# Kernel optimization log

Hardware: AMD Instinct MI355X
Metric: run time of the kernel (lower is better)

## Reference

```python
import jax, jax.numpy as jnp
import numpy as np

B, S, D, H = 4, 2048, 1024, 16
HD = D // H  # head_dim = 64


def setup_inputs() -> dict:
    key = jax.random.key(0)
    k1, k2, k3 = jax.random.split(key, 3)
    scale = 0.02
    return {
        "hidden_states": jax.random.normal(k1, (B, S, D), dtype=jnp.float32),
        "W_attn": jax.random.normal(k2, (D, 3 * D), dtype=jnp.float32) * scale,
        "b_attn": jnp.zeros((3 * D,), dtype=jnp.float32),
        "W_proj": jax.random.normal(k3, (D, D), dtype=jnp.float32) * scale,
        "b_proj": jnp.zeros((D,), dtype=jnp.float32),
    }


def reference(hidden_states, W_attn, b_attn, W_proj, b_proj):
    b, s, d = hidden_states.shape
    qkv = hidden_states @ W_attn + b_attn  # [B,S,3D]
    q, k, v = jnp.split(qkv, 3, axis=-1)
    # [B,S,D] -> [B,H,S,hd]
    def to_heads(x):
        return x.reshape(b, s, H, HD).transpose(0, 2, 1, 3)
    q, k, v = to_heads(q), to_heads(k), to_heads(v)
    scores = jnp.einsum("bhqd,bhkd->bhqk", q, k) / jnp.sqrt(jnp.float32(HD))
    causal = jnp.tril(jnp.ones((s, s), dtype=bool))  # [S,S]
    scores = jnp.where(causal[None, None], scores, jnp.float32(-jnp.inf))
    probs = jax.nn.softmax(scores, axis=-1)  # dropout p=0 -> identity (eval)
    out = jnp.einsum("bhqk,bhkd->bhqd", probs, v)  # [B,H,S,hd]
    out = out.transpose(0, 2, 1, 3).reshape(b, s, d)
    return out @ W_proj + b_proj
```

## Files before the change

kernel.cpp:

```cpp
#include <hip/hip_runtime.h>
#include <hip/hip_bf16.h>


typedef float f32x4 __attribute__((ext_vector_type(4)));
typedef __bf16 bf16x8 __attribute__((ext_vector_type(8)));
typedef unsigned short u16x8 __attribute__((ext_vector_type(8)));
typedef unsigned short u16x4 __attribute__((ext_vector_type(4)));

static constexpr int Sq = 2048, Dm = 1024, HD = 64, N3 = 3072;
static constexpr int Mrows = 4 * Sq;
static constexpr float SM_SCALE = 0.18033688011112042f;
static constexpr float SM_BIAS  = -11.541560327111707f;

__device__ __forceinline__ float bf2f(unsigned short u) {
  union { unsigned u32; float f; } x; x.u32 = ((unsigned)u) << 16; return x.f;
}
__device__ __forceinline__ unsigned short f2bf(float f) {
  return __builtin_bit_cast(unsigned short, (__bf16)f);
}
__device__ __forceinline__ f32x4 mfma16(u16x8 a, u16x8 b, f32x4 c) {
  return __builtin_amdgcn_mfma_f32_16x16x32_bf16(
      __builtin_bit_cast(bf16x8, a), __builtin_bit_cast(bf16x8, b), c, 0, 0, 0);
}

__global__ __launch_bounds__(256) void cvt_k(
    const float* __restrict__ in, unsigned short* __restrict__ out, int n) {
  int stride = gridDim.x * 256 * 4;
  for (int i = (blockIdx.x * 256 + threadIdx.x) * 4; i < n; i += stride) {
    f32x4 v = *reinterpret_cast<const f32x4*>(&in[i]);
    u16x4 o;
    #pragma unroll
    for (int j = 0; j < 4; j++) o[j] = f2bf(v[j]);
    *reinterpret_cast<u16x4*>(&out[i]) = o;
  }
}

__global__ __launch_bounds__(256) void tcvt_k(
    const float* __restrict__ in, unsigned short* __restrict__ out,
    int R, int C) {
  __shared__ float tile[32][33];
  int c0 = blockIdx.x * 32, r0 = blockIdx.y * 32;
  int tx = threadIdx.x & 31, ty = threadIdx.x >> 5;
  #pragma unroll
  for (int i = 0; i < 32; i += 8)
    tile[ty + i][tx] = in[(size_t)(r0 + ty + i) * C + c0 + tx];
  __syncthreads();
  #pragma unroll
  for (int i = 0; i < 32; i += 8)
    out[(size_t)(c0 + ty + i) * R + r0 + tx] = f2bf(tile[tx][ty + i]);
}

template <bool OUT_F32>
__global__ __launch_bounds__(256) void gemm_bt(
    const unsigned short* __restrict__ A, const unsigned short* __restrict__ Bt,
    const float* __restrict__ bias, void* __restrict__ Cout,
    int Md, int Nd, int Kd) {
  __shared__ unsigned short Asm[128 * 32];
  __shared__ unsigned short Bsm[128 * 32];
  int t = threadIdx.x;
  int wave = t >> 6, lane = t & 63;
  int lrow = lane & 15, lq = lane >> 4;
  int wr = wave >> 1, wc = wave & 1;
  int bm = blockIdx.y * 128, bn = blockIdx.x * 128;
  f32x4 acc[4][4] = {};

  for (int k0 = 0; k0 < Kd; k0 += 32) {
    __syncthreads();
    #pragma unroll
    for (int c = 0; c < 2; c++) {
      int e = c * 2048 + t * 8;
      int row = e >> 5, col = e & 31;
      const unsigned short* ga = A + (size_t)(bm + row) * Kd + k0 + col;
      const unsigned short* gb = Bt + (size_t)(bn + row) * Kd + k0 + col;
      __builtin_amdgcn_global_load_lds(
          (const __attribute__((address_space(1))) void*)ga,
          (__attribute__((address_space(3))) void*)((char*)Asm + c * 4096 + wave * 1024),
          16, 0, 0);
      __builtin_amdgcn_global_load_lds(
          (const __attribute__((address_space(1))) void*)gb,
          (__attribute__((address_space(3))) void*)((char*)Bsm + c * 4096 + wave * 1024),
          16, 0, 0);
    }
    __syncthreads();

    u16x8 af[4], bfr[4];
    #pragma unroll
    for (int m = 0; m < 4; m++)
      af[m] = *reinterpret_cast<const u16x8*>(&Asm[(wr * 64 + m * 16 + lrow) * 32 + lq * 8]);
    #pragma unroll
    for (int n = 0; n < 4; n++)
      bfr[n] = *reinterpret_cast<const u16x8*>(&Bsm[(wc * 64 + n * 16 + lrow) * 32 + lq * 8]);
    #pragma unroll
    for (int m = 0; m < 4; m++)
      #pragma unroll
      for (int n = 0; n < 4; n++)
        acc[m][n] = mfma16(af[m], bfr[n], acc[m][n]);
  }

  #pragma unroll
  for (int n = 0; n < 4; n++) {
    int col = bn + wc * 64 + n * 16 + lrow;
    float bv = bias[col];
    #pragma unroll
    for (int m = 0; m < 4; m++) {
      #pragma unroll
      for (int j = 0; j < 4; j++) {
        int row = bm + wr * 64 + m * 16 + lq * 4 + j;
        if constexpr (OUT_F32)
          ((float*)Cout)[(size_t)row * Nd + col] = acc[m][n][j] + bv;
        else
          ((unsigned short*)Cout)[(size_t)row * Nd + col] = f2bf(acc[m][n][j] + bv);
      }
    }
  }
}

__global__ __launch_bounds__(256) void attn_k(
    const unsigned short* __restrict__ qkv,
    unsigned short* __restrict__ ao) {
  int bh = blockIdx.y;
  int b = bh >> 4, h = bh & 15;
  int t = threadIdx.x, wave = t >> 6, lane = t & 63;
  int lrow = lane & 15, lq = lane >> 4;

  __shared__ unsigned short Kl[2][64][72];
  __shared__ unsigned short Vt[2][64][72];
  __shared__ unsigned short Pl[4][16][72];

  const size_t base = (size_t)b * Sq * N3;
  const unsigned short* Kbase = qkv + base + Dm + h * HD;
  const unsigned short* Vbase = qkv + base + 2 * Dm + h * HD;

  int irow = t >> 2, icol = (t & 3) * 16;
  int vd = lane, vkb = wave;

  u16x8 ones;
  #pragma unroll
  for (int j = 0; j < 8; j++) ones[j] = 0x3F80;

  u16x8 kr0, kr1, vr0, vr1;
  auto prefetch = [&](int kv) {
    const unsigned short* kp = Kbase + (size_t)(kv + irow) * N3 + icol;
    kr0 = *reinterpret_cast<const u16x8*>(kp);
    kr1 = *reinterpret_cast<const u16x8*>(kp + 8);
    const unsigned short* vp = Vbase + (size_t)kv * N3 + vd;
    #pragma unroll
    for (int i = 0; i < 8; i++) {
      vr0[i] = vp[(size_t)(vkb * 8 + i) * N3];
      vr1[i] = vp[(size_t)(32 + vkb * 8 + i) * N3];
    }
  };

  #pragma unroll 1
  for (int pass = 0; pass < 2; ++pass) {
    int qb = pass ? (int)blockIdx.x : 15 - (int)blockIdx.x;
    int q0 = qb * 128;
    int ntiles = 2 * qb + 2;
    int rw0 = q0 + wave * 32;

    u16x8 qf[2][2];
    #pragma unroll
    for (int m = 0; m < 2; m++) {
      const unsigned short* qp =
          qkv + base + (size_t)(rw0 + m * 16 + lrow) * N3 + h * HD + lq * 8;
      u16x8 r0 = *reinterpret_cast<const u16x8*>(qp);
      u16x8 r1 = *reinterpret_cast<const u16x8*>(qp + 32);
      #pragma unroll
      for (int j = 0; j < 8; j++) {
        qf[m][0][j] = f2bf(SM_SCALE * bf2f(r0[j]));
        qf[m][1][j] = f2bf(SM_SCALE * bf2f(r1[j]));
      }
    }

    f32x4 oacc[2][4] = {};
    f32x4 dacc[2] = {};

    if (pass == 0) prefetch(0);

    #pragma unroll 1
    for (int kt = 0; kt < ntiles; ++kt) {
      int kv = kt * 64, bsel = kt & 1;
      *reinterpret_cast<u16x8*>(&Kl[bsel][irow][icol]) = kr0;
      *reinterpret_cast<u16x8*>(&Kl[bsel][irow][icol + 8]) = kr1;
      *reinterpret_cast<u16x8*>(&Vt[bsel][vd][vkb * 8]) = vr0;
      *reinterpret_cast<u16x8*>(&Vt[bsel][vd][32 + vkb * 8]) = vr1;
      if (kt + 1 < ntiles) prefetch(kv + 64);
      else if (pass == 0) prefetch(0);
      __syncthreads();

      u16x8 kf0[4], kf1[4];
      #pragma unroll
      for (int ct = 0; ct < 4; ct++) {
        kf0[ct] = *reinterpret_cast<const u16x8*>(&Kl[bsel][ct * 16 + lrow][lq * 8]);
        kf1[ct] = *reinterpret_cast<const u16x8*>(&Kl[bsel][ct * 16 + lrow][32 + lq * 8]);
      }
      f32x4 sacc[2][4];
      #pragma unroll
      for (int m = 0; m < 2; m++)
        #pragma unroll
        for (int ct = 0; ct < 4; ct++)
          sacc[m][ct] = f32x4{SM_BIAS, SM_BIAS, SM_BIAS, SM_BIAS};
      __builtin_amdgcn_s_setprio(1);
      #pragma unroll
      for (int m = 0; m < 2; m++)
        #pragma unroll
        for (int ct = 0; ct < 4; ct++) {
          sacc[m][ct] = mfma16(kf0[ct], qf[m][0], sacc[m][ct]);
          sacc[m][ct] = mfma16(kf1[ct], qf[m][1], sacc[m][ct]);
        }
      __builtin_amdgcn_s_setprio(0);

      u16x8 vf0[4], vf1[4];
      #pragma unroll
      for (int ht = 0; ht < 4; ht++) {
        vf0[ht] = *reinterpret_cast<const u16x8*>(&Vt[bsel][ht * 16 + lrow][lq * 8]);
        vf1[ht] = *reinterpret_cast<const u16x8*>(&Vt[bsel][ht * 16 + lrow][32 + lq * 8]);
      }

      #pragma unroll
      for (int m = 0; m < 2; m++) {
        int rwm = rw0 + m * 16;
        bool need_mask = kv + 63 > rwm;
        int dlim = rwm - kv + lrow;
        #pragma unroll
        for (int ct = 0; ct < 4; ct++) {
          u16x4 o;
          #pragma unroll
          for (int j = 0; j < 4; j++) {
            float e = exp2f(sacc[m][ct][j]);
            if (need_mask) e = (16 * ct + 4 * lq + j <= dlim) ? e : 0.f;
            o[j] = f2bf(e);
          }
          *reinterpret_cast<u16x4*>(&Pl[wave][lrow][16 * ct + 4 * lq]) = o;
        }

        u16x8 pa0 = *reinterpret_cast<const u16x8*>(&Pl[wave][lrow][lq * 8]);
        u16x8 pa1 = *reinterpret_cast<const u16x8*>(&Pl[wave][lrow][32 + lq * 8]);
        __builtin_amdgcn_s_setprio(1);
        dacc[m] = mfma16(pa0, ones, dacc[m]);
        dacc[m] = mfma16(pa1, ones, dacc[m]);
        #pragma unroll
        for (int ht = 0; ht < 4; ht++) {
          oacc[m][ht] = mfma16(pa0, vf0[ht], oacc[m][ht]);
          oacc[m][ht] = mfma16(pa1, vf1[ht], oacc[m][ht]);
        }
        __builtin_amdgcn_s_setprio(0);
      }
    }

    #pragma unroll
    for (int m = 0; m < 2; m++) {
      float inv[4];
      #pragma unroll
      for (int j = 0; j < 4; j++) inv[j] = __builtin_amdgcn_rcpf(dacc[m][j]);
      #pragma unroll
      for (int ht = 0; ht < 4; ht++)
        #pragma unroll
        for (int j = 0; j < 4; j++) {
          int rg = rw0 + m * 16 + lq * 4 + j;
          float v = oacc[m][ht][j] * inv[j];
          ao[(size_t)(b * Sq + rg) * Dm + h * HD + ht * 16 + lrow] = f2bf(v);
        }
    }
  }
}

extern "C" void kernel_launch(void* const* d_in, const int* in_sizes, int n_in,
                              void* d_out, int out_size, void* d_ws, size_t ws_size,
                              hipStream_t stream) {
  const float* hs = (const float*)d_in[0];
  const float* Wa = (const float*)d_in[1];
  const float* ba = (const float*)d_in[2];
  const float* Wp = (const float*)d_in[3];
  const float* bp = (const float*)d_in[4];
  float* out = (float*)d_out;

  char* ws = (char*)d_ws;
  unsigned short* QKV = (unsigned short*)ws;
  unsigned short* WaT = (unsigned short*)(ws + 50331648);
  unsigned short* AO  = (unsigned short*)(ws + 50331648);
  unsigned short* WpT = (unsigned short*)ws;
  unsigned short* hsB = (unsigned short*)d_out;

  cvt_k<<<2048, 256, 0, stream>>>(hs, hsB, Mrows * Dm);
  tcvt_k<<<dim3(96, 32), 256, 0, stream>>>(Wa, WaT, 1024, 3072);
  gemm_bt<false><<<dim3(24, 64), 256, 0, stream>>>(hsB, WaT, ba, QKV, Mrows, N3, Dm);
  attn_k<<<dim3(8, 64), 256, 0, stream>>>(QKV, AO);
  tcvt_k<<<dim3(32, 32), 256, 0, stream>>>(Wp, WpT, 1024, 1024);
  gemm_bt<true><<<dim3(8, 64), 256, 0, stream>>>(AO, WpT, bp, out, Mrows, Dm, Dm);
}
```

Before: 211.2 us.

## Double attention query tile to 256 rows with 8 waves splitting K/V staging

```diff
diff --git a/kernel.cpp b/kernel.cpp
--- a/kernel.cpp
+++ b/kernel.cpp
@@ -115,60 +115,65 @@
   }
 }
 
-__global__ __launch_bounds__(256) void attn_k(
+__global__ __launch_bounds__(512, 4) void attn_k(
     const unsigned short* __restrict__ qkv,
     unsigned short* __restrict__ ao) {
-  int bh = blockIdx.y;
+  int bh = ((int)blockIdx.x & 7) + 8 * (int)blockIdx.y;
+  int qp = (int)blockIdx.x >> 3;
   int b = bh >> 4, h = bh & 15;
   int t = threadIdx.x, wave = t >> 6, lane = t & 63;
   int lrow = lane & 15, lq = lane >> 4;
 
   __shared__ unsigned short Kl[2][64][72];
   __shared__ unsigned short Vt[2][64][72];
-  __shared__ unsigned short Pl[4][16][72];
+  __shared__ unsigned short Pl[8][16][72];
 
   const size_t base = (size_t)b * Sq * N3;
   const unsigned short* Kbase = qkv + base + Dm + h * HD;
   const unsigned short* Vbase = qkv + base + 2 * Dm + h * HD;
 
+  bool stageK = wave < 4;
   int irow = t >> 2, icol = (t & 3) * 16;
-  int vd = lane, vkb = wave;
+  int vd = t & 63, vkb = (t >> 6) & 3;
 
   u16x8 ones;
   #pragma unroll
   for (int j = 0; j < 8; j++) ones[j] = 0x3F80;
 
-  u16x8 kr0, kr1, vr0, vr1;
+  u16x8 r0, r1;
   auto prefetch = [&](int kv) {
-    const unsigned short* kp = Kbase + (size_t)(kv + irow) * N3 + icol;
-    kr0 = *reinterpret_cast<const u16x8*>(kp);
-    kr1 = *reinterpret_cast<const u16x8*>(kp + 8);
-    const unsigned short* vp = Vbase + (size_t)kv * N3 + vd;
-    #pragma unroll
-    for (int i = 0; i < 8; i++) {
-      vr0[i] = vp[(size_t)(vkb * 8 + i) * N3];
-      vr1[i] = vp[(size_t)(32 + vkb * 8 + i) * N3];
+    if (stageK) {
+      const unsigned short* kp = Kbase + (size_t)(kv + irow) * N3 + icol;
+      r0 = *reinterpret_cast<const u16x8*>(kp);
+      r1 = *reinterpret_cast<const u16x8*>(kp + 8);
+    } else {
+      const unsigned short* vp = Vbase + (size_t)kv * N3 + vd;
+      #pragma unroll
+      for (int i = 0; i < 8; i++) {
+        r0[i] = vp[(size_t)(vkb * 8 + i) * N3];
+        r1[i] = vp[(size_t)(32 + vkb * 8 + i) * N3];
+      }
     }
   };
 
   #pragma unroll 1
   for (int pass = 0; pass < 2; ++pass) {
-    int qb = pass ? (int)blockIdx.x : 15 - (int)blockIdx.x;
-    int q0 = qb * 128;
-    int ntiles = 2 * qb + 2;
+    int qb = pass ? qp : 7 - qp;
+    int q0 = qb * 256;
+    int ntiles = 4 * qb + 4;
     int rw0 = q0 + wave * 32;
 
     u16x8 qf[2][2];
     #pragma unroll
     for (int m = 0; m < 2; m++) {
-      const unsigned short* qp =
+      const unsigned short* qp_ =
           qkv + base + (size_t)(rw0 + m * 16 + lrow) * N3 + h * HD + lq * 8;
-      u16x8 r0 = *reinterpret_cast<const u16x8*>(qp);
-      u16x8 r1 = *reinterpret_cast<const u16x8*>(qp + 32);
+      u16x8 a0 = *reinterpret_cast<const u16x8*>(qp_);
+      u16x8 a1 = *reinterpret_cast<const u16x8*>(qp_ + 32);
       #pragma unroll
       for (int j = 0; j < 8; j++) {
-        qf[m][0][j] = f2bf(SM_SCALE * bf2f(r0[j]));
-        qf[m][1][j] = f2bf(SM_SCALE * bf2f(r1[j]));
+        qf[m][0][j] = f2bf(SM_SCALE * bf2f(a0[j]));
+        qf[m][1][j] = f2bf(SM_SCALE * bf2f(a1[j]));
       }
     }
 
@@ -180,10 +185,13 @@
     #pragma unroll 1
     for (int kt = 0; kt < ntiles; ++kt) {
       int kv = kt * 64, bsel = kt & 1;
-      *reinterpret_cast<u16x8*>(&Kl[bsel][irow][icol]) = kr0;
-      *reinterpret_cast<u16x8*>(&Kl[bsel][irow][icol + 8]) = kr1;
-      *reinterpret_cast<u16x8*>(&Vt[bsel][vd][vkb * 8]) = vr0;
-      *reinterpret_cast<u16x8*>(&Vt[bsel][vd][32 + vkb * 8]) = vr1;
+      if (stageK) {
+        *reinterpret_cast<u16x8*>(&Kl[bsel][irow][icol]) = r0;
+        *reinterpret_cast<u16x8*>(&Kl[bsel][irow][icol + 8]) = r1;
+      } else {
+        *reinterpret_cast<u16x8*>(&Vt[bsel][vd][vkb * 8]) = r0;
+        *reinterpret_cast<u16x8*>(&Vt[bsel][vd][32 + vkb * 8]) = r1;
+      }
       if (kt + 1 < ntiles) prefetch(kv + 64);
       else if (pass == 0) prefetch(0);
       __syncthreads();
@@ -285,7 +293,7 @@
   cvt_k<<<2048, 256, 0, stream>>>(hs, hsB, Mrows * Dm);
   tcvt_k<<<dim3(96, 32), 256, 0, stream>>>(Wa, WaT, 1024, 3072);
   gemm_bt<false><<<dim3(24, 64), 256, 0, stream>>>(hsB, WaT, ba, QKV, Mrows, N3, Dm);
-  attn_k<<<dim3(8, 64), 256, 0, stream>>>(QKV, AO);
+  attn_k<<<dim3(32, 8), 512, 0, stream>>>(QKV, AO);
   tcvt_k<<<dim3(32, 32), 256, 0, stream>>>(Wp, WpT, 1024, 1024);
   gemm_bt<true><<<dim3(8, 64), 256, 0, stream>>>(AO, WpT, bp, out, Mrows, Dm, Dm);
 }
```

New measurement: 357.4 us. +69.2%, slower.
